# Performance work log

Measured on AMD Instinct MI355X. Metric: run time of the kernel, lower is better.

Reference implementation:

```python
import jax, jax.numpy as jnp
import numpy as np

B, S, D = 8, 2048, 512
MINF = 20000.0  # matches tf code's -20000.0 mask constant


def setup_inputs() -> dict:
    key = jax.random.key(0)
    k1, k2, k3 = jax.random.split(key, 3)
    x1 = jax.random.normal(k1, (B, S, D), dtype=jnp.float32)
    x2 = jax.random.normal(k2, (B, S, D), dtype=jnp.float32)
    # glorot_normal init for the learned (S, S) positional kernel
    std = np.sqrt(2.0 / (S + S)).astype(np.float32)
    kernel = jax.random.normal(k3, (S, S), dtype=jnp.float32) * std
    return {"x1": x1, "x2": x2, "kernel": kernel}


def reference(x1, x2, kernel):
    S_ = kernel.shape[0]
    # tf.matmul(kernel, inputs[i]) broadcasts (S,S) @ (B,S,D) -> (B,S,D)
    h1 = jnp.einsum('st,btd->bsd', kernel, x1)
    h2 = jnp.einsum('st,btd->bsd', kernel, x2)
    # att_scores: (B, S, S)
    scores = jnp.einsum('bsd,btd->bst', h1, h2)
    d_k = jnp.asarray(S_, dtype=scores.dtype) ** 0.5
    # upper_m[i,j] = -20000 for j > i (strictly upper), else 0; added BEFORE scaling
    row = jnp.arange(S_)
    mask = jnp.where(row[None, :] > row[:, None], -MINF, 0.0).astype(scores.dtype)
    attn = jax.nn.softmax((scores + mask) / d_k, axis=-1)
    # note: output attends over h1 (not h2), as in the original code
    return jnp.einsum('bst,btd->bsd', attn, h1)
```

## Files before the change

### kernel.cpp

```cpp
#include <hip/hip_runtime.h>
#include <hip/hip_bf16.h>

#define S_DIM 2048
#define D_DIM 512
#define B_DIM 8
#define SCALE 0.02209708691207961f

typedef __hip_bfloat16 bf16;
typedef short bf16x8 __attribute__((ext_vector_type(8)));
typedef float f32x4 __attribute__((ext_vector_type(4)));

__device__ __forceinline__ unsigned short f2b(float f) {
  __hip_bfloat16 h = __float2bfloat16(f);
  return __builtin_bit_cast(unsigned short, h);
}
__device__ __forceinline__ float b2f(unsigned short s) {
  return __bfloat162float(__builtin_bit_cast(__hip_bfloat16, s));
}

__device__ __forceinline__ void load_lds16(const void* g, void* l) {
  __builtin_amdgcn_global_load_lds((const __attribute__((address_space(1))) void*)g,
                                   (__attribute__((address_space(3))) void*)l, 16, 0, 0);
}

__global__ void convert_k(const float* __restrict__ in, bf16* __restrict__ out, int n8) {
  int i = blockIdx.x * blockDim.x + threadIdx.x;
  if (i >= n8) return;
  const float4* p = (const float4*)in;
  float4 a = p[2 * i], b = p[2 * i + 1];
  bf16x8 r;
  r[0] = f2b(a.x); r[1] = f2b(a.y); r[2] = f2b(a.z); r[3] = f2b(a.w);
  r[4] = f2b(b.x); r[5] = f2b(b.y); r[6] = f2b(b.z); r[7] = f2b(b.w);
  ((bf16x8*)out)[i] = r;
}

__global__ void tr_f2b64(const float* __restrict__ x1, const float* __restrict__ x2,
                         bf16* __restrict__ out) {
  __shared__ unsigned short t[64][66];
  const int z = blockIdx.z;
  const float* in = (z < 8 ? x1 : x2) + (size_t)(z & 7) * (S_DIM * D_DIM);
  bf16* ob = out + (size_t)z * (size_t)(D_DIM * S_DIM);
  const int r0 = blockIdx.y * 64;
  const int c0 = blockIdx.x * 64;
  const int tid = threadIdx.x;
  const int lr = tid >> 6, lc = tid & 63;
#pragma unroll
  for (int i = 0; i < 16; i++) {
    int r = i * 4 + lr;
    t[lc][r] = f2b(in[(size_t)(r0 + r) * D_DIM + c0 + lc]);
  }
  __syncthreads();
  const int dl = tid >> 4, tq = tid & 15;
#pragma unroll
  for (int j = 0; j < 4; j++) {
    int d = j * 16 + dl;
    const unsigned short* p = &t[d][tq * 4];
    uint2 u;
    u.x = (unsigned)p[0] | ((unsigned)p[1] << 16);
    u.y = (unsigned)p[2] | ((unsigned)p[3] << 16);
    *(uint2*)(ob + (size_t)(c0 + d) * S_DIM + r0 + tq * 4) = u;
  }
}

__global__ void tr_b2b64(const bf16* __restrict__ in, bf16* __restrict__ out) {
  __shared__ unsigned short t[64][66];
  const int z = blockIdx.z;
  const bf16* ib = in + (size_t)z * (S_DIM * D_DIM);
  bf16* ob = out + (size_t)z * (S_DIM * D_DIM);
  const int r0 = blockIdx.y * 64;
  const int c0 = blockIdx.x * 64;
  const int tid = threadIdx.x;
  const int lr = tid >> 5, cp = tid & 31;
#pragma unroll
  for (int i = 0; i < 8; i++) {
    int r = i * 8 + lr;
    unsigned v = *(const unsigned*)(ib + (size_t)(r0 + r) * D_DIM + c0 + cp * 2);
    t[cp * 2][r] = (unsigned short)(v & 0xffff);
    t[cp * 2 + 1][r] = (unsigned short)(v >> 16);
  }
  __syncthreads();
  const int dl = tid >> 4, tq = tid & 15;
#pragma unroll
  for (int j = 0; j < 4; j++) {
    int d = j * 16 + dl;
    const unsigned short* p = &t[d][tq * 4];
    uint2 u;
    u.x = (unsigned)p[0] | ((unsigned)p[1] << 16);
    u.y = (unsigned)p[2] | ((unsigned)p[3] << 16);
    *(uint2*)(ob + (size_t)(c0 + d) * S_DIM + r0 + tq * 4) = u;
  }
}

__global__ __launch_bounds__(512, 2) void gemm_h(
    const bf16* __restrict__ A, const bf16* __restrict__ X, bf16* __restrict__ H) {
  extern __shared__ char smem[];
  const int pid = blockIdx.x;
  const int mt = pid & 7;
  const int r_ = pid >> 3;
  const int ntile = r_ & 1;
  const int item = r_ >> 1;
  const int m0 = mt * 256, n0 = ntile * 256;
  const bf16* Xi = X + (size_t)item * (D_DIM * S_DIM);
  bf16* Hi = H + (size_t)item * (S_DIM * D_DIM);

  const int tid = threadIdx.x;
  const int w = tid >> 6, L = tid & 63;
  const int l15 = L & 15, lhi = L >> 4;
  const int wr = w >> 2, wn = w & 3;

  const int srow = tid >> 2;
  const int sslot = ((tid & 3) ^ ((tid >> 3) & 3)) * 8;
  const bf16* pA[2];
  const bf16* pB[2];
#pragma unroll
  for (int ld = 0; ld < 2; ld++) {
    pA[ld] = A + (size_t)(m0 + ld * 128 + srow) * 2048 + sslot;
    pB[ld] = Xi + (size_t)(n0 + ld * 128 + srow) * 2048 + sslot;
  }

  char* A0 = smem;          char* A1 = smem + 16384;  char* A2 = smem + 32768;
  char* B0 = smem + 49152;  char* B1 = smem + 65536;  char* B2 = smem + 81920;

  auto stage = [&](int t2, char* dA, char* dB) {
#pragma unroll
    for (int ld = 0; ld < 2; ld++)
      load_lds16(pA[ld] + t2 * 32, dA + ld * 8192 + w * 1024);
#pragma unroll
    for (int ld = 0; ld < 2; ld++)
      load_lds16(pB[ld] + t2 * 32, dB + ld * 8192 + w * 1024);
  };

  const int xo = (lhi ^ ((l15 >> 1) & 3)) << 4;
  int offA[8], offB[4];
#pragma unroll
  for (int m = 0; m < 8; m++) offA[m] = (wr * 128 + m * 16 + l15) * 64 + xo;
#pragma unroll
  for (int n = 0; n < 4; n++) offB[n] = (wn * 64 + n * 16 + l15) * 64 + xo;

  f32x4 acc[8][4];
#pragma unroll
  for (int m = 0; m < 8; m++)
#pragma unroll
    for (int n = 0; n < 4; n++) acc[m][n] = (f32x4){0, 0, 0, 0};

  stage(0, A0, B0);
  stage(1, A1, B1);

#pragma unroll 1
  for (int t = 0; t < 64; ++t) {
    if (t < 63) asm volatile("s_waitcnt vmcnt(4)" ::: "memory");
    else        asm volatile("s_waitcnt vmcnt(0)" ::: "memory");
    __builtin_amdgcn_s_barrier();
    asm volatile("" ::: "memory");
    if (t < 62) stage(t + 2, A2, B2);

    bf16x8 af[8], bfv[4];
#pragma unroll
    for (int m = 0; m < 8; m++) af[m] = *(const bf16x8*)(A0 + offA[m]);
#pragma unroll
    for (int n = 0; n < 4; n++) bfv[n] = *(const bf16x8*)(B0 + offB[n]);
    __builtin_amdgcn_s_setprio(1);
#pragma unroll
    for (int m = 0; m < 8; m++)
#pragma unroll
      for (int n = 0; n < 4; n++)
        acc[m][n] = __builtin_amdgcn_mfma_f32_16x16x32_bf16(bfv[n], af[m], acc[m][n], 0, 0, 0);
    __builtin_amdgcn_s_setprio(0);

    char* tA = A0; A0 = A1; A1 = A2; A2 = tA;
    char* tB = B0; B0 = B1; B1 = B2; B2 = tB;
  }

#pragma unroll
  for (int m = 0; m < 8; m++) {
    int grow = m0 + wr * 128 + m * 16 + l15;
#pragma unroll
    for (int n = 0; n < 4; n++) {
      int gcol = n0 + wn * 64 + n * 16 + lhi * 4;
      uint2 u;
      u.x = ((unsigned)f2b(acc[m][n][1]) << 16) | f2b(acc[m][n][0]);
      u.y = ((unsigned)f2b(acc[m][n][3]) << 16) | f2b(acc[m][n][2]);
      *(uint2*)(Hi + (size_t)grow * D_DIM + gcol) = u;
    }
  }
}

__global__ __launch_bounds__(512, 2) void gemm_score(
    const bf16* __restrict__ H1, const bf16* __restrict__ H2,
    bf16* __restrict__ E, float* __restrict__ rowsum) {
  extern __shared__ char smem[];
  const int pid = blockIdx.x;
  const int b = pid & 7;
  const int tri = pid >> 3;
  int mt = (int)((sqrtf(8.0f * (float)tri + 1.0f) - 1.0f) * 0.5f);
  while ((mt + 1) * (mt + 2) / 2 <= tri) mt++;
  while (mt * (mt + 1) / 2 > tri) mt--;
  const int nt = tri - mt * (mt + 1) / 2;
  const int m0 = mt * 256, n0 = nt * 256;
  const bool diag = (mt == nt);
  const bf16* Ab = H1 + (size_t)b * S_DIM * D_DIM;
  const bf16* Bb = H2 + (size_t)b * S_DIM * D_DIM;
  bf16* Eb = E + (size_t)b * S_DIM * S_DIM;
  float* rs = rowsum + b * S_DIM;

  const int tid = threadIdx.x;
  const int w = tid >> 6, L = tid & 63;
  const int l15 = L & 15, lhi = L >> 4;
  const int wr = w >> 2, wn = w & 3;

  const int srow = tid >> 2;
  const int sslot = ((tid & 3) ^ ((tid >> 3) & 3)) * 8;
  const bf16* pA[2];
  const bf16* pB[2];
#pragma unroll
  for (int ld = 0; ld < 2; ld++) {
    pA[ld] = Ab + (size_t)(m0 + ld * 128 + srow) * D_DIM + sslot;
    pB[ld] = Bb + (size_t)(n0 + ld * 128 + srow) * D_DIM + sslot;
  }

  char* A0 = smem;          char* A1 = smem + 16384;  char* A2 = smem + 32768;
  char* B0 = smem + 49152;  char* B1 = smem + 65536;  char* B2 = smem + 81920;

  auto stage = [&](int t2, char* dA, char* dB) {
#pragma unroll
    for (int ld = 0; ld < 2; ld++)
      load_lds16(pA[ld] + t2 * 32, dA + ld * 8192 + w * 1024);
#pragma unroll
    for (int ld = 0; ld < 2; ld++)
      load_lds16(pB[ld] + t2 * 32, dB + ld * 8192 + w * 1024);
  };

  const int xo = (lhi ^ ((l15 >> 1) & 3)) << 4;
  int offA[8], offB[4];
#pragma unroll
  for (int m = 0; m < 8; m++) offA[m] = (wr * 128 + m * 16 + l15) * 64 + xo;
#pragma unroll
  for (int n = 0; n < 4; n++) offB[n] = (wn * 64 + n * 16 + l15) * 64 + xo;

  f32x4 acc[8][4];
#pragma unroll
  for (int m = 0; m < 8; m++)
#pragma unroll
    for (int n = 0; n < 4; n++) acc[m][n] = (f32x4){0, 0, 0, 0};

  stage(0, A0, B0);
  stage(1, A1, B1);

#pragma unroll 1
  for (int t = 0; t < 16; ++t) {
    if (t < 15) asm volatile("s_waitcnt vmcnt(4)" ::: "memory");
    else        asm volatile("s_waitcnt vmcnt(0)" ::: "memory");
    __builtin_amdgcn_s_barrier();
    asm volatile("" ::: "memory");
    if (t < 14) stage(t + 2, A2, B2);

    bf16x8 af[8], bfv[4];
#pragma unroll
    for (int m = 0; m < 8; m++) af[m] = *(const bf16x8*)(A0 + offA[m]);
#pragma unroll
    for (int n = 0; n < 4; n++) bfv[n] = *(const bf16x8*)(B0 + offB[n]);
    __builtin_amdgcn_s_setprio(1);
#pragma unroll
    for (int m = 0; m < 8; m++)
#pragma unroll
      for (int n = 0; n < 4; n++)
        acc[m][n] = __builtin_amdgcn_mfma_f32_16x16x32_bf16(bfv[n], af[m], acc[m][n], 0, 0, 0);
    __builtin_amdgcn_s_setprio(0);

    char* tA = A0; A0 = A1; A1 = A2; A2 = tA;
    char* tB = B0; B0 = B1; B1 = B2; B2 = tB;
  }

#pragma unroll
  for (int m = 0; m < 8; m++) {
    int sg = m0 + wr * 128 + m * 16 + l15;
    float rp = 0.0f;
#pragma unroll
    for (int n = 0; n < 4; n++) {
      int tg0 = n0 + wn * 64 + n * 16 + lhi * 4;
      unsigned short e[4];
#pragma unroll
      for (int r = 0; r < 4; r++) {
        float v = (!diag || (tg0 + r) <= sg) ? __expf(acc[m][n][r] * SCALE) : 0.0f;
        e[r] = f2b(v);
        rp += b2f(e[r]);
      }
      uint2 u;
      u.x = ((unsigned)e[1] << 16) | e[0];
      u.y = ((unsigned)e[3] << 16) | e[2];
      *(uint2*)(Eb + (size_t)sg * S_DIM + tg0) = u;
    }
    rp += __shfl_xor(rp, 16);
    rp += __shfl_xor(rp, 32);
    if (lhi == 0) atomicAdd(rs + sg, rp);
  }
}

__global__ __launch_bounds__(256, 2) void gemm_pv(
    const bf16* __restrict__ E, const bf16* __restrict__ H1T,
    const float* __restrict__ rowsum, float* __restrict__ out) {
  extern __shared__ char smem[];
  const int pid = blockIdx.x;
  const int b = pid & 7;
  const int r_ = pid >> 3;
  const int nt = r_ & 3;
  const int mb = r_ >> 2;
  const int mt = (mb < 8) ? 2 * mb : 31 - 2 * mb;
  const int m0 = mt * 128, n0 = nt * 128;
  const int NT = (mt + 1) * 4;
  const bf16* Ab = E + (size_t)b * S_DIM * S_DIM + (size_t)m0 * S_DIM;
  const bf16* Bb = H1T + (size_t)b * D_DIM * S_DIM + (size_t)n0 * S_DIM;
  const float* rs = rowsum + b * S_DIM;
  float* Cb = out + (size_t)b * S_DIM * D_DIM;

  const int tid = threadIdx.x;
  const int w = tid >> 6, L = tid & 63;
  const int l15 = L & 15, lhi = L >> 4;
  const int wr = w >> 1, wc = w & 1;

  const int srow = tid >> 2;
  const int sslot = ((tid & 3) ^ ((tid >> 3) & 3)) * 8;
  const bf16* pA[2];
  const bf16* pB[2];
#pragma unroll
  for (int ld = 0; ld < 2; ld++) {
    pA[ld] = Ab + (size_t)(ld * 64 + srow) * S_DIM + sslot;
    pB[ld] = Bb + (size_t)(ld * 64 + srow) * S_DIM + sslot;
  }

  char* A0 = smem;          char* A1 = smem + 8192;   char* A2 = smem + 16384;
  char* B0 = smem + 24576;  char* B1 = smem + 32768;  char* B2 = smem + 40960;

  auto stage = [&](int t2, char* dA, char* dB) {
#pragma unroll
    for (int ld = 0; ld < 2; ld++)
      load_lds16(pA[ld] + t2 * 32, dA + ld * 4096 + w * 1024);
#pragma unroll
    for (int ld = 0; ld < 2; ld++)
      load_lds16(pB[ld] + t2 * 32, dB + ld * 4096 + w * 1024);
  };

  const int xo = (lhi ^ ((l15 >> 1) & 3)) << 4;
  int offA[4], offB[4];
#pragma unroll
  for (int m = 0; m < 4; m++) offA[m] = (wr * 64 + m * 16 + l15) * 64 + xo;
#pragma unroll
  for (int n = 0; n < 4; n++) offB[n] = (wc * 64 + n * 16 + l15) * 64 + xo;

  f32x4 acc[4][4];
#pragma unroll
  for (int m = 0; m < 4; m++)
#pragma unroll
    for (int n = 0; n < 4; n++) acc[m][n] = (f32x4){0, 0, 0, 0};

  stage(0, A0, B0);
  stage(1, A1, B1);

#pragma unroll 1
  for (int t = 0; t < NT; ++t) {
    if (t < NT - 1) asm volatile("s_waitcnt vmcnt(4)" ::: "memory");
    else            asm volatile("s_waitcnt vmcnt(0)" ::: "memory");
    __builtin_amdgcn_s_barrier();
    asm volatile("" ::: "memory");
    if (t + 2 < NT) stage(t + 2, A2, B2);

    bf16x8 af[4], bfv[4];
#pragma unroll
    for (int m = 0; m < 4; m++) af[m] = *(const bf16x8*)(A0 + offA[m]);
#pragma unroll
    for (int n = 0; n < 4; n++) bfv[n] = *(const bf16x8*)(B0 + offB[n]);
    __builtin_amdgcn_s_setprio(1);
#pragma unroll
    for (int m = 0; m < 4; m++)
#pragma unroll
      for (int n = 0; n < 4; n++)
        acc[m][n] = __builtin_amdgcn_mfma_f32_16x16x32_bf16(bfv[n], af[m], acc[m][n], 0, 0, 0);
    __builtin_amdgcn_s_setprio(0);

    char* tA = A0; A0 = A1; A1 = A2; A2 = tA;
    char* tB = B0; B0 = B1; B1 = B2; B2 = tB;
  }

#pragma unroll
  for (int m = 0; m < 4; m++) {
    int sg = m0 + wr * 64 + m * 16 + l15;
    float inv = 1.0f / rs[sg];
#pragma unroll
    for (int n = 0; n < 4; n++) {
      int gcol = n0 + wc * 64 + n * 16 + lhi * 4;
      float4 o;
      o.x = acc[m][n][0] * inv;
      o.y = acc[m][n][1] * inv;
      o.z = acc[m][n][2] * inv;
      o.w = acc[m][n][3] * inv;
      *(float4*)(Cb + (size_t)sg * D_DIM + gcol) = o;
    }
  }
}

extern "C" void kernel_launch(void* const* d_in, const int* in_sizes, int n_in,
                              void* d_out, int out_size, void* d_ws, size_t ws_size,
                              hipStream_t stream) {
  const float* x1 = (const float*)d_in[0];
  const float* x2 = (const float*)d_in[1];
  const float* km = (const float*)d_in[2];
  float* out = (float*)d_out;
  char* ws = (char*)d_ws;
  bf16* E    = (bf16*)(ws);
  bf16* Kbf  = (bf16*)(ws);
  bf16* x1t  = (bf16*)(ws + (8ull << 20));
  bf16* h1n  = (bf16*)(ws + (64ull << 20));
  bf16* h2n  = (bf16*)(ws + (80ull << 20));
  bf16* h1t  = (bf16*)(ws + (96ull << 20));
  float* rowsum = (float*)(ws + (112ull << 20));

  convert_k<<<2048, 256, 0, stream>>>(km, Kbf, (S_DIM * S_DIM) / 8);
  tr_f2b64<<<dim3(8, 32, 16), 256, 0, stream>>>(x1, x2, x1t);
  gemm_h<<<256, 512, 98304, stream>>>(Kbf, x1t, h1n);
  tr_b2b64<<<dim3(8, 32, 8), 256, 0, stream>>>(h1n, h1t);
  hipMemsetAsync(rowsum, 0, B_DIM * S_DIM * sizeof(float), stream);
  gemm_score<<<288, 512, 98304, stream>>>(h1n, h2n, E, rowsum);
  gemm_pv<<<512, 256, 49152, stream>>>(E, h1t, rowsum, out);
}
```

Baseline: 173.9 us.

## Restructure gemm_h into K=64 double-buffered ping-pong with quarter-tile MFMA phases

Rewrites the gemm_h main loop to use K-steps of 64 (32 iterations), double-buffered 128KB LDS tiles split into halves, and four quarter MFMA phases separated by barriers, interleaving LDS reads and global-to-LDS staging of the next tiles between phases. Occupancy drops to one block per CU (launch bounds 512,1). The aim is to reduce per-iteration barrier and waitcnt overhead and to overlap loads with MFMA work in a ping-pong schedule, which needs more LDS and fewer resident waves. Extra barriers per iteration and the lower occupancy may offset the gains.

New measurement: 174.4 us. No clear change (+0.3%).

```diff
diff --git a/kernel.cpp b/kernel.cpp
--- a/kernel.cpp
+++ b/kernel.cpp
@@ -91,7 +91,7 @@
   }
 }
 
-__global__ __launch_bounds__(512, 2) void gemm_h(
+__global__ __launch_bounds__(512, 1) void gemm_h(
     const bf16* __restrict__ A, const bf16* __restrict__ X, bf16* __restrict__ H) {
   extern __shared__ char smem[];
   const int pid = blockIdx.x;
@@ -100,7 +100,8 @@
   const int ntile = r_ & 1;
   const int item = r_ >> 1;
   const int m0 = mt * 256, n0 = ntile * 256;
-  const bf16* Xi = X + (size_t)item * (D_DIM * S_DIM);
+  const bf16* Asrc = A + (size_t)m0 * S_DIM;
+  const bf16* Bsrc = X + (size_t)item * (D_DIM * S_DIM) + (size_t)n0 * S_DIM;
   bf16* Hi = H + (size_t)item * (S_DIM * D_DIM);
 
   const int tid = threadIdx.x;
@@ -108,34 +109,51 @@
   const int l15 = L & 15, lhi = L >> 4;
   const int wr = w >> 2, wn = w & 3;
 
-  const int srow = tid >> 2;
-  const int sslot = ((tid & 3) ^ ((tid >> 3) & 3)) * 8;
-  const bf16* pA[2];
-  const bf16* pB[2];
-#pragma unroll
-  for (int ld = 0; ld < 2; ld++) {
-    pA[ld] = A + (size_t)(m0 + ld * 128 + srow) * 2048 + sslot;
-    pB[ld] = Xi + (size_t)(n0 + ld * 128 + srow) * 2048 + sslot;
-  }
-
-  char* A0 = smem;          char* A1 = smem + 16384;  char* A2 = smem + 32768;
-  char* B0 = smem + 49152;  char* B1 = smem + 65536;  char* B2 = smem + 81920;
-
-  auto stage = [&](int t2, char* dA, char* dB) {
-#pragma unroll
-    for (int ld = 0; ld < 2; ld++)
-      load_lds16(pA[ld] + t2 * 32, dA + ld * 8192 + w * 1024);
-#pragma unroll
-    for (int ld = 0; ld < 2; ld++)
-      load_lds16(pB[ld] + t2 * 32, dB + ld * 8192 + w * 1024);
-  };
-
-  const int xo = (lhi ^ ((l15 >> 1) & 3)) << 4;
-  int offA[8], offB[4];
-#pragma unroll
-  for (int m = 0; m < 8; m++) offA[m] = (wr * 128 + m * 16 + l15) * 64 + xo;
-#pragma unroll
-  for (int n = 0; n < 4; n++) offB[n] = (wn * 64 + n * 16 + l15) * 64 + xo;
+  const int sr8 = L >> 3;
+  const int sslot = ((L & 7) ^ sr8) * 8;
+  const bf16* pA[2][2];
+  const bf16* pB[2][2];
+#pragma unroll
+  for (int h = 0; h < 2; h++)
+#pragma unroll
+    for (int ld = 0; ld < 2; ld++) {
+      pA[h][ld] = Asrc + (size_t)(h * 128 + w * 16 + ld * 8 + sr8) * S_DIM + sslot;
+      pB[h][ld] = Bsrc + (size_t)(h * 128 + w * 16 + ld * 8 + sr8) * S_DIM + sslot;
+    }
+
+  auto stageA = [&](int t2, int half) {
+    char* d = smem + ((t2 & 1) << 15) + (half << 14) + w * 2048;
+#pragma unroll
+    for (int ld = 0; ld < 2; ld++) load_lds16(pA[half][ld] + t2 * 64, d + ld * 1024);
+  };
+  auto stageB = [&](int t2, int half) {
+    char* d = smem + 65536 + ((t2 & 1) << 15) + (half << 14) + w * 2048;
+#pragma unroll
+    for (int ld = 0; ld < 2; ld++) load_lds16(pB[half][ld] + t2 * 64, d + ld * 1024);
+  };
+
+  const int xsw = l15 & 7;
+  const int cK0 = (lhi ^ xsw) << 4;
+  const int cK1 = ((4 + lhi) ^ xsw) << 4;
+
+  bf16x8 af[4][2], bfr[2][2];
+  auto readA = [&](int buf, int mh) {
+    const char* base = smem + (buf << 15) + (wr << 14) + mh * 8192 + l15 * 128;
+#pragma unroll
+    for (int m = 0; m < 4; m++) {
+      af[m][0] = *(const bf16x8*)(base + m * 2048 + cK0);
+      af[m][1] = *(const bf16x8*)(base + m * 2048 + cK1);
+    }
+  };
+  auto readB = [&](int buf, int nh) {
+    const char* base = smem + 65536 + (buf << 15) + ((wn >> 1) << 14) + (wn & 1) * 8192 +
+                       nh * 4096 + l15 * 128;
+#pragma unroll
+    for (int n = 0; n < 2; n++) {
+      bfr[n][0] = *(const bf16x8*)(base + n * 2048 + cK0);
+      bfr[n][1] = *(const bf16x8*)(base + n * 2048 + cK1);
+    }
+  };
 
   f32x4 acc[8][4];
 #pragma unroll
@@ -143,32 +161,51 @@
 #pragma unroll
     for (int n = 0; n < 4; n++) acc[m][n] = (f32x4){0, 0, 0, 0};
 
-  stage(0, A0, B0);
-  stage(1, A1, B1);
-
-#pragma unroll 1
-  for (int t = 0; t < 64; ++t) {
-    if (t < 63) asm volatile("s_waitcnt vmcnt(4)" ::: "memory");
-    else        asm volatile("s_waitcnt vmcnt(0)" ::: "memory");
+  auto mfmaQ = [&](int mh, int nh) {
+    __builtin_amdgcn_s_setprio(1);
+#pragma unroll
+    for (int kk = 0; kk < 2; kk++)
+#pragma unroll
+      for (int m = 0; m < 4; m++)
+#pragma unroll
+        for (int n = 0; n < 2; n++)
+          acc[mh * 4 + m][nh * 2 + n] = __builtin_amdgcn_mfma_f32_16x16x32_bf16(
+              bfr[n][kk], af[m][kk], acc[mh * 4 + m][nh * 2 + n], 0, 0, 0);
+    __builtin_amdgcn_s_setprio(0);
+  };
+  auto bar = [&] {
+    asm volatile("" ::: "memory");
     __builtin_amdgcn_s_barrier();
     asm volatile("" ::: "memory");
-    if (t < 62) stage(t + 2, A2, B2);
-
-    bf16x8 af[8], bfv[4];
-#pragma unroll
-    for (int m = 0; m < 8; m++) af[m] = *(const bf16x8*)(A0 + offA[m]);
-#pragma unroll
-    for (int n = 0; n < 4; n++) bfv[n] = *(const bf16x8*)(B0 + offB[n]);
-    __builtin_amdgcn_s_setprio(1);
-#pragma unroll
-    for (int m = 0; m < 8; m++)
-#pragma unroll
-      for (int n = 0; n < 4; n++)
-        acc[m][n] = __builtin_amdgcn_mfma_f32_16x16x32_bf16(bfv[n], af[m], acc[m][n], 0, 0, 0);
-    __builtin_amdgcn_s_setprio(0);
-
-    char* tA = A0; A0 = A1; A1 = A2; A2 = tA;
-    char* tB = B0; B0 = B1; B1 = B2; B2 = tB;
+  };
+  auto lgkm0 = [&] { asm volatile("s_waitcnt lgkmcnt(0)" ::: "memory"); };
+
+  const int NT = 32;
+  stageA(0, 0); stageA(0, 1); stageB(0, 0); stageB(0, 1);
+  stageA(1, 0); stageA(1, 1);
+  asm volatile("s_waitcnt vmcnt(4)" ::: "memory");
+  bar();
+
+#pragma unroll 1
+  for (int t = 0; t < NT; ++t) {
+    const int buf = t & 1;
+    const bool s1 = (t + 1 < NT);
+    const bool s2 = (t + 2 < NT);
+    readA(buf, 0); readB(buf, 0);
+    if (s1) stageB(t + 1, 0);
+    bar(); lgkm0(); mfmaQ(0, 0); bar();
+    readB(buf, 1);
+    if (s1) stageB(t + 1, 1);
+    bar(); lgkm0(); mfmaQ(0, 1); bar();
+    readA(buf, 1); readB(buf, 0);
+    if (s2) stageA(t + 2, 0);
+    bar(); lgkm0(); mfmaQ(1, 0); bar();
+    readB(buf, 1);
+    if (s2) stageA(t + 2, 1);
+    bar(); lgkm0(); mfmaQ(1, 1);
+    if (s2) asm volatile("s_waitcnt vmcnt(4)" ::: "memory");
+    else    asm volatile("s_waitcnt vmcnt(0)" ::: "memory");
+    bar();
   }
 
 #pragma unroll
@@ -416,7 +453,7 @@
 
   convert_k<<<2048, 256, 0, stream>>>(km, Kbf, (S_DIM * S_DIM) / 8);
   tr_f2b64<<<dim3(8, 32, 16), 256, 0, stream>>>(x1, x2, x1t);
-  gemm_h<<<256, 512, 98304, stream>>>(Kbf, x1t, h1n);
+  gemm_h<<<256, 512, 131072, stream>>>(Kbf, x1t, h1n);
   tr_b2b64<<<dim3(8, 32, 8), 256, 0, stream>>>(h1n, h1t);
   hipMemsetAsync(rowsum, 0, B_DIM * S_DIM * sizeof(float), stream);
   gemm_score<<<288, 512, 98304, stream>>>(h1n, h2n, E, rowsum);
```
